# Kernel tuning notes

Measured on AMD Instinct MI355X. Metric: run time of the kernel, lower is better.

Reference implementation:

```python
import jax, jax.numpy as jnp
import numpy as np

NUM_NODES = 15000


def _gcn_conv(x, W, b, src, dst, norm, num_nodes):
    # PyG GCNConv: x' = D^-1/2 (A + I) D^-1/2 (x W) + b
    h = x @ W                                   # [N, out]
    msg = h[src] * norm[:, None]                # gather + scale per edge
    out = jax.ops.segment_sum(msg, dst, num_segments=num_nodes)
    return out + b


def setup_inputs() -> dict:
    key = jax.random.key(0)
    ks = jax.random.split(key, 12)
    T = 100000
    E = 200000
    inp = {
        "x": jax.random.normal(ks[0], (NUM_NODES, 768), jnp.float32),
        "r_emb": jax.random.normal(ks[1], (T, 768), jnp.float32),
        "W1": jax.random.normal(ks[2], (768, 10), jnp.float32) * 0.05,
        "b1": jax.random.normal(ks[3], (10,), jnp.float32) * 0.05,
        "W2": jax.random.normal(ks[4], (10, 128), jnp.float32) * 0.05,
        "b2": jax.random.normal(ks[5], (128,), jnp.float32) * 0.05,
        "W_ih": jax.random.normal(ks[6], (512, 1024), jnp.float32) * 0.03,
        "W_hh": jax.random.normal(ks[7], (512, 128), jnp.float32) * 0.03,
        "b_ih": jax.random.normal(ks[8], (512,), jnp.float32) * 0.03,
        "b_hh": jax.random.normal(ks[9], (512,), jnp.float32) * 0.03,
        "edge_index": jax.random.randint(ks[10], (2, E), 0, NUM_NODES).astype(jnp.int64),
        "triples": jax.random.randint(ks[11], (T, 3), 0, NUM_NODES).astype(jnp.int64),
    }
    return inp


def reference(x, r_emb, W1, b1, W2, b2, W_ih, W_hh, b_ih, b_hh, edge_index, triples):
    N = x.shape[0]
    H = 128  # lstm hidden size
    # --- add self loops, symmetric GCN normalization ---
    loop = jnp.arange(N, dtype=edge_index.dtype)
    src = jnp.concatenate([edge_index[0], loop])
    dst = jnp.concatenate([edge_index[1], loop])
    deg = jax.ops.segment_sum(jnp.ones_like(dst, jnp.float32), dst, num_segments=N)
    dinv = jnp.where(deg > 0, jax.lax.rsqrt(deg), 0.0)
    norm = dinv[src] * dinv[dst]                      # [E+N]
    # --- 2-layer GCN ---
    h = jax.nn.relu(_gcn_conv(x, W1, b1, src, dst, norm, N))   # [N, 10]
    z = _gcn_conv(h, W2, b2, src, dst, norm, N)                # [N, 128]
    # --- per-triple LSTM scoring, batched (seq_len=1, zero init state) ---
    hvec = z[triples[:, 0]]                           # [T, 128]
    tvec = z[triples[:, 2]]                           # [T, 128]
    feat = jnp.concatenate([hvec, r_emb, tvec], axis=-1)       # [T, 1024]
    gates = feat @ W_ih.T + (b_ih + b_hh)             # [T, 512]; h0=0 so W_hh term vanishes
    i_g, f_g, g_g, o_g = jnp.split(gates, 4, axis=-1)  # torch gate order i,f,g,o
    c = jax.nn.sigmoid(i_g) * jnp.tanh(g_g)           # c0 = 0 -> forget term drops
    out = jax.nn.sigmoid(o_g) * jnp.tanh(c)           # [T, 128]
    score = jax.nn.sigmoid(jnp.sum(out, axis=-1))     # [T]
    return score
```

## Files before the change

kernel.cpp:

```cpp
#include <hip/hip_runtime.h>

#define NF 768
#define D1 10
#define D2 128
#define BM 64

typedef __attribute__((ext_vector_type(8))) short bf16x8;
typedef __attribute__((ext_vector_type(16))) float f32x16;

static __device__ __forceinline__ float sigf(float v){ return 1.0f/(1.0f+__expf(-v)); }
static __device__ __forceinline__ float tanhfast(float v){ return 2.0f/(1.0f+__expf(-2.0f*v)) - 1.0f; }
static __device__ __forceinline__ short f2bf(float f){
    unsigned u = __float_as_uint(f);
    u += 0x7fffu + ((u>>16)&1u);
    return (short)(u>>16);
}

__global__ void k_deg(const int* __restrict__ dst, int* __restrict__ cnt, int E){
    int e = blockIdx.x*256 + threadIdx.x;
    if(e<E) atomicAdd(&cnt[dst[e]], 1);
}

__global__ __launch_bounds__(256) void k_scan(const int* __restrict__ cnt,
                                              int* __restrict__ rowptr, int* __restrict__ rowcur,
                                              float* __restrict__ dinv, int N, int E){
    __shared__ int part[256];
    int t = threadIdx.x;
    int C = (N+255)/256;
    int lo = t*C, hi = lo+C; if(hi>N) hi=N; if(lo>N) lo=N;
    int s=0;
    for(int i=lo;i<hi;i++) s += cnt[i];
    part[t]=s;
    __syncthreads();
    if(t==0){
        int run=0;
        for(int i=0;i<256;i++){ int v=part[i]; part[i]=run; run+=v; }
        rowptr[N]=E;
    }
    __syncthreads();
    int run = part[t];
    for(int i=lo;i<hi;i++){
        rowptr[i]=run; rowcur[i]=run; run += cnt[i];
        dinv[i] = rsqrtf((float)cnt[i] + 1.0f);
    }
}

__global__ void k_fill(const int* __restrict__ src, const int* __restrict__ dst,
                       const float* __restrict__ dinv, int* __restrict__ rowcur,
                       int* __restrict__ esrc, float* __restrict__ enorm, int E){
    int e = blockIdx.x*256 + threadIdx.x;
    if(e>=E) return;
    int s=src[e], d=dst[e];
    int pos = atomicAdd(&rowcur[d], 1);
    esrc[pos]=s;
    enorm[pos]=dinv[s]*dinv[d];
}

__global__ __launch_bounds__(256) void k_h1(const float* __restrict__ x,
                                            const float* __restrict__ W1,
                                            float* __restrict__ h1, int N){
    __shared__ float wt[D1*NF];
    for(int idx=threadIdx.x; idx<NF*D1; idx+=256){
        int k=idx/D1, c=idx-k*D1;
        wt[c*NF+k]=W1[idx];
    }
    __syncthreads();
    int row = blockIdx.x*4 + (threadIdx.x>>6);
    int lane = threadIdx.x&63;
    if(row>=N) return;
    const float4* xr = (const float4*)(x + (size_t)row*NF);
    float acc[D1];
#pragma unroll
    for(int c=0;c<D1;c++) acc[c]=0.f;
#pragma unroll
    for(int i=0;i<3;i++){
        float4 v = xr[lane + 64*i];
#pragma unroll
        for(int c=0;c<D1;c++){
            float4 w = *(const float4*)&wt[c*NF + (lane+64*i)*4];
            acc[c] += v.x*w.x + v.y*w.y + v.z*w.z + v.w*w.w;
        }
    }
#pragma unroll
    for(int c=0;c<D1;c++){
        float v=acc[c];
#pragma unroll
        for(int off=32;off;off>>=1) v += __shfl_down(v,off,64);
        acc[c]=v;
    }
    if(lane==0){
#pragma unroll
        for(int c=0;c<D1;c++) h1[(size_t)row*D1+c]=acc[c];
    }
}

__global__ __launch_bounds__(256) void k_gath1(const float* __restrict__ h1,
        const int* __restrict__ rowptr, const int* __restrict__ esrc,
        const float* __restrict__ enorm, const float* __restrict__ dinv,
        const float* __restrict__ b1, float* __restrict__ h, int N){
    int node = blockIdx.x*4 + (threadIdx.x>>6);
    int lane = threadIdx.x&63;
    if(node>=N) return;
    int e0=rowptr[node], e1=rowptr[node+1];
    float acc[D1];
#pragma unroll
    for(int c=0;c<D1;c++) acc[c]=0.f;
    for(int e=e0+lane; e<e1; e+=64){
        int s=esrc[e]; float w=enorm[e];
        const float* hr = h1 + (size_t)s*D1;
#pragma unroll
        for(int c=0;c<D1;c++) acc[c] += hr[c]*w;
    }
    if(lane==0){
        float di=dinv[node], d2=di*di;
        const float* hr = h1 + (size_t)node*D1;
#pragma unroll
        for(int c=0;c<D1;c++) acc[c] += hr[c]*d2;
    }
#pragma unroll
    for(int c=0;c<D1;c++){
        float v=acc[c];
#pragma unroll
        for(int off=32;off;off>>=1) v += __shfl_down(v,off,64);
        acc[c]=v;
    }
    if(lane==0){
#pragma unroll
        for(int c=0;c<D1;c++){
            float v = acc[c] + b1[c];
            h[(size_t)node*D1+c] = v>0.f ? v : 0.f;
        }
    }
}

__global__ __launch_bounds__(128) void k_hz(const float* __restrict__ h,
                                            const float* __restrict__ W2,
                                            float* __restrict__ hz, int N){
    __shared__ float w2s[D1*D2];
    int j = threadIdx.x;
    for(int i=j;i<D1*D2;i+=128) w2s[i]=W2[i];
    __syncthreads();
    int n = blockIdx.x;
    if(n>=N) return;
    const float* hr = h + (size_t)n*D1;
    float acc=0.f;
#pragma unroll
    for(int k=0;k<D1;k++) acc += hr[k]*w2s[k*D2+j];
    hz[(size_t)n*D2+j]=acc;
}

__global__ __launch_bounds__(128) void k_gath2(const float* __restrict__ hz,
        const int* __restrict__ rowptr, const int* __restrict__ esrc,
        const float* __restrict__ enorm, const float* __restrict__ dinv,
        const float* __restrict__ b2, ushort* __restrict__ zb, int N){
    int n = blockIdx.x;
    int c = threadIdx.x;
    int e0 = rowptr[n], e1 = rowptr[n+1];
    float di = dinv[n];
    float acc = hz[(size_t)n*D2+c]*di*di + b2[c];
    int e = e0;
    for(; e+1<e1; e+=2){
        int s0=esrc[e], s1=esrc[e+1];
        float w0=enorm[e], w1=enorm[e+1];
        acc += hz[(size_t)s0*D2+c]*w0 + hz[(size_t)s1*D2+c]*w1;
    }
    if(e<e1) acc += hz[(size_t)esrc[e]*D2+c]*enorm[e];
    zb[(size_t)n*D2+c] = (ushort)f2bf(acc);
}

__global__ void k_wimgB(const float* __restrict__ Wih, ushort* __restrict__ img){
    int gid = blockIdx.x*256 + threadIdx.x;
    if(gid >= 12*64*64) return;
    int l = gid & 63;
    int ks16 = (gid>>6) & 63;
    int f = gid >> 12;
    int dd = l & 31, kb = l>>5;
    int wn = f/3, gi = f - wn*3;
    int gbase = (gi==0)?0:((gi==1)?256:384);
    int wrow = gbase + wn*32 + dd;
    int k = ks16*16 + kb*8;
    const float* p = Wih + (size_t)wrow*1024 + k;
    float4 v0=*(const float4*)p, v1=*(const float4*)(p+4);
    bf16x8 o;
    o[0]=f2bf(v0.x); o[1]=f2bf(v0.y); o[2]=f2bf(v0.z); o[3]=f2bf(v0.w);
    o[4]=f2bf(v1.x); o[5]=f2bf(v1.y); o[6]=f2bf(v1.z); o[7]=f2bf(v1.w);
    *(bf16x8*)(img + (size_t)gid*8) = o;
}

static __device__ __forceinline__ void stage_chunk(ushort* __restrict__ buf, int ch,
        int tid, int t0, int T, const float* __restrict__ remb,
        const ushort* __restrict__ zb, const int* __restrict__ trip){
    int row = tid>>2, q = tid&3;
    int tc = t0+row; if(tc>=T) tc=T-1;
    int xr = row&7;
    ushort* lrow = buf + row*256;
    const size_t rb = (size_t)tc*NF;
#pragma unroll
    for(int j=0;j<8;j++){
        int s = q + 4*j;
        int G = ch*32 + s;
        if(G < 16){
            const ushort* zrow = zb + (size_t)trip[3*tc]*D2;
            *(int4*)(lrow + (s^xr)*8) = *(const int4*)(zrow + G*8);
        } else if(G < 112){
            int g = G-16;
            const float* p = remb + rb + (size_t)g*8;
            float4 v0=*(const float4*)p, v1=*(const float4*)(p+4);
            bf16x8 o;
            o[0]=f2bf(v0.x); o[1]=f2bf(v0.y); o[2]=f2bf(v0.z); o[3]=f2bf(v0.w);
            o[4]=f2bf(v1.x); o[5]=f2bf(v1.y); o[6]=f2bf(v1.z); o[7]=f2bf(v1.w);
            *(bf16x8*)(lrow + (s^xr)*8) = o;
        } else {
            const ushort* zrow = zb + (size_t)trip[3*tc+2]*D2;
            *(int4*)(lrow + (s^xr)*8) = *(const int4*)(zrow + (G-112)*8);
        }
    }
}

__global__ __launch_bounds__(256,2) void k_big(
    const float* __restrict__ remb, const ushort* __restrict__ img,
    const ushort* __restrict__ zb, const float* __restrict__ b_ih,
    const float* __restrict__ b_hh, const int* __restrict__ trip,
    float* __restrict__ score, int T)
{
    __shared__ ushort Abuf[2][64*256];
    int tid=threadIdx.x, lane=tid&63, wn=tid>>6;
    int l31=lane&31, lh=lane>>5;
    int t0=blockIdx.x*BM;

    const ushort* wb0 = img + ((size_t)(wn*3+0)*64*64 + lane)*8;
    const ushort* wb1 = img + ((size_t)(wn*3+1)*64*64 + lane)*8;
    const ushort* wb2 = img + ((size_t)(wn*3+2)*64*64 + lane)*8;
    const int base0 = l31*256;
    const int base1 = (32+l31)*256;
    const int xorm = l31&7;

    f32x16 acc[2][3];
    const f32x16 zer = {0,0,0,0,0,0,0,0,0,0,0,0,0,0,0,0};
#pragma unroll
    for(int m=0;m<2;m++)
#pragma unroll
        for(int g=0;g<3;g++) acc[m][g]=zer;

    stage_chunk(Abuf[0], 0, tid, t0, T, remb, zb, trip);
    __syncthreads();

    for(int ch=0; ch<4; ++ch){
        ushort* cur = Abuf[ch&1];
        if(ch<3) stage_chunk(Abuf[(ch+1)&1], ch+1, tid, t0, T, remb, zb, trip);
        bf16x8 qb[2][3], pa[2][2];
#pragma unroll
        for(int p=0;p<2;p++){
            int ks = ch*16 + p;
            qb[p][0]=*(const bf16x8*)(wb0+(size_t)ks*512);
            qb[p][1]=*(const bf16x8*)(wb1+(size_t)ks*512);
            qb[p][2]=*(const bf16x8*)(wb2+(size_t)ks*512);
            pa[p][0]=*(const bf16x8*)&cur[base0 + ((p*2+lh)^xorm)*8];
            pa[p][1]=*(const bf16x8*)&cur[base1 + ((p*2+lh)^xorm)*8];
        }
#pragma unroll
        for(int c=0;c<16;c++){
            int bs=c&1;
            bf16x8 a0=pa[bs][0], a1=pa[bs][1];
            bf16x8 b0=qb[bs][0], b1=qb[bs][1], b2=qb[bs][2];
            if(c+2<16){
                int ks = ch*16 + c+2;
                qb[bs][0]=*(const bf16x8*)(wb0+(size_t)ks*512);
                qb[bs][1]=*(const bf16x8*)(wb1+(size_t)ks*512);
                qb[bs][2]=*(const bf16x8*)(wb2+(size_t)ks*512);
                pa[bs][0]=*(const bf16x8*)&cur[base0 + (((c+2)*2+lh)^xorm)*8];
                pa[bs][1]=*(const bf16x8*)&cur[base1 + (((c+2)*2+lh)^xorm)*8];
            }
            acc[0][0]=__builtin_amdgcn_mfma_f32_32x32x16_bf16(a0,b0,acc[0][0],0,0,0);
            acc[0][1]=__builtin_amdgcn_mfma_f32_32x32x16_bf16(a0,b1,acc[0][1],0,0,0);
            acc[0][2]=__builtin_amdgcn_mfma_f32_32x32x16_bf16(a0,b2,acc[0][2],0,0,0);
            acc[1][0]=__builtin_amdgcn_mfma_f32_32x32x16_bf16(a1,b0,acc[1][0],0,0,0);
            acc[1][1]=__builtin_amdgcn_mfma_f32_32x32x16_bf16(a1,b1,acc[1][1],0,0,0);
            acc[1][2]=__builtin_amdgcn_mfma_f32_32x32x16_bf16(a1,b2,acc[1][2],0,0,0);
        }
        __syncthreads();
    }

    float* rowsum = (float*)&Abuf[0][0];
    if(tid<BM) rowsum[tid]=0.f;
    __syncthreads();
    int d = wn*32+l31;
    float bi=b_ih[d]+b_hh[d];
    float bg=b_ih[256+d]+b_hh[256+d];
    float bo=b_ih[384+d]+b_hh[384+d];
#pragma unroll
    for(int m=0;m<2;m++){
#pragma unroll
        for(int r=0;r<16;r++){
            int row = m*32 + (r&3)+8*(r>>2)+4*lh;
            float ig = acc[m][0][r] + bi;
            float gg = acc[m][1][r] + bg;
            float og = acc[m][2][r] + bo;
            float cc = sigf(ig)*tanhfast(gg);
            float ov = sigf(og)*tanhfast(cc);
#pragma unroll
            for(int off=1; off<32; off<<=1) ov += __shfl_xor(ov, off, 64);
            if(l31==0) atomicAdd(&rowsum[row], ov);
        }
    }
    __syncthreads();
    if(tid < BM){
        int t = t0 + tid;
        if(t < T) score[t] = sigf(rowsum[tid]);
    }
}

extern "C" void kernel_launch(void* const* d_in, const int* in_sizes, int n_in,
                              void* d_out, int out_size, void* d_ws, size_t ws_size,
                              hipStream_t stream){
    const float* x    = (const float*)d_in[0];
    const float* remb = (const float*)d_in[1];
    const float* W1   = (const float*)d_in[2];
    const float* b1   = (const float*)d_in[3];
    const float* W2   = (const float*)d_in[4];
    const float* b2   = (const float*)d_in[5];
    const float* Wih  = (const float*)d_in[6];
    const float* b_ih = (const float*)d_in[8];
    const float* b_hh = (const float*)d_in[9];
    const int*   ei   = (const int*)d_in[10];
    const int*   trip = (const int*)d_in[11];
    float* score = (float*)d_out;

    const int N = in_sizes[0]/NF;
    const int E = in_sizes[10]/2;
    const int T = in_sizes[11]/3;
    const int* src = ei;
    const int* dst = ei + E;

    float* ws = (float*)d_ws;
    size_t o = 0;
    ushort* img  = (ushort*)(ws+o); o += (size_t)12*64*64*8/2;
    ushort* zb   = (ushort*)(ws+o); o += (size_t)N*D2/2;
    int*   cnt    = (int*)(ws+o);   o += (size_t)((N+8)&~7);
    int*   rowptr = (int*)(ws+o);   o += (size_t)((N+8)&~7);
    int*   rowcur = (int*)(ws+o);   o += (size_t)((N+8)&~7);
    int*   esrc   = (int*)(ws+o);   o += (size_t)E;
    float* enorm  = ws+o;           o += (size_t)E;
    float* dinv   = ws+o;           o += (size_t)((N+7)&~7);
    float* h1     = ws+o;           o += (size_t)N*D1;
    float* hbuf   = ws+o;           o += (size_t)N*D1;
    float* hz     = ws+o;           o += (size_t)N*D2;
    (void)ws_size; (void)n_in; (void)out_size;

    hipMemsetAsync(cnt, 0, (size_t)N*sizeof(int), stream);

    k_wimgB<<<dim3((12*64*64+255)/256), dim3(256), 0, stream>>>(Wih, img);
    k_deg  <<<dim3((E+255)/256), dim3(256), 0, stream>>>(dst, cnt, E);
    k_scan <<<dim3(1), dim3(256), 0, stream>>>(cnt, rowptr, rowcur, dinv, N, E);
    k_fill <<<dim3((E+255)/256), dim3(256), 0, stream>>>(src, dst, dinv, rowcur, esrc, enorm, E);
    k_h1   <<<dim3((N+3)/4), dim3(256), 0, stream>>>(x, W1, h1, N);
    k_gath1<<<dim3((N+3)/4), dim3(256), 0, stream>>>(h1, rowptr, esrc, enorm, dinv, b1, hbuf, N);
    k_hz   <<<dim3(N), dim3(128), 0, stream>>>(hbuf, W2, hz, N);
    k_gath2<<<dim3(N), dim3(128), 0, stream>>>(hz, rowptr, esrc, enorm, dinv, b2, zb, N);
    k_big  <<<dim3((T+BM-1)/BM), dim3(256), 0, stream>>>(remb, img, zb, b_ih, b_hh, trip, score, T);
}
```

Measured before the change: 324.3 us.

## Split A-tile staging into async register loads overlapped with MFMA, reorder LDS layout

The staging of each A chunk is split into an issue phase (global loads into registers) and a write phase (bf16 convert and LDS store). These are interleaved with the two halves of the MFMA loop, so global latency is hidden behind compute. The LDS layout changes to a fragment-major order so each lane reads contiguous 16 bytes with no XOR swizzle. The weight prefetch distance grows from 2 to 4 k-steps and crosses chunk boundaries, and s_setprio raises wave priority during the MFMA bursts. In exchange, register pressure rises from the pending buffers and the deeper B prefetch, which could hurt occupancy under launch_bounds(256,2).

```diff
diff --git a/kernel.cpp b/kernel.cpp
--- a/kernel.cpp
+++ b/kernel.cpp
@@ -187,32 +187,45 @@
     *(bf16x8*)(img + (size_t)gid*8) = o;
 }
 
-static __device__ __forceinline__ void stage_chunk(ushort* __restrict__ buf, int ch,
+struct PendG { float4 lo, hi; };
+
+static __device__ __forceinline__ void issue_groups(PendG* __restrict__ pend, int ch1, int jbase,
         int tid, int t0, int T, const float* __restrict__ remb,
         const ushort* __restrict__ zb, const int* __restrict__ trip){
     int row = tid>>2, q = tid&3;
     int tc = t0+row; if(tc>=T) tc=T-1;
-    int xr = row&7;
-    ushort* lrow = buf + row*256;
-    const size_t rb = (size_t)tc*NF;
-#pragma unroll
-    for(int j=0;j<8;j++){
-        int s = q + 4*j;
-        int G = ch*32 + s;
+#pragma unroll
+    for(int j=0;j<4;j++){
+        int gl = q + 4*(jbase+j);
+        int G = ch1*32 + gl;
         if(G < 16){
-            const ushort* zrow = zb + (size_t)trip[3*tc]*D2;
-            *(int4*)(lrow + (s^xr)*8) = *(const int4*)(zrow + G*8);
+            pend[j].lo = *(const float4*)(zb + (size_t)trip[3*tc]*D2 + G*8);
         } else if(G < 112){
-            int g = G-16;
-            const float* p = remb + rb + (size_t)g*8;
-            float4 v0=*(const float4*)p, v1=*(const float4*)(p+4);
+            const float* p = remb + (size_t)tc*NF + (size_t)(G-16)*8;
+            pend[j].lo = *(const float4*)p;
+            pend[j].hi = *(const float4*)(p+4);
+        } else {
+            pend[j].lo = *(const float4*)(zb + (size_t)trip[3*tc+2]*D2 + (size_t)(G-112)*8);
+        }
+    }
+}
+
+static __device__ __forceinline__ void write_groups(ushort* __restrict__ buf,
+        const PendG* __restrict__ pend, int ch1, int jbase, int tid){
+    int row = tid>>2, q = tid&3;
+    int mb = row>>5, r31 = row&31;
+#pragma unroll
+    for(int j=0;j<4;j++){
+        int gl = q + 4*(jbase+j);
+        int G = ch1*32 + gl;
+        int slot = ((mb*16 + (gl>>1))*64 + r31 + 32*(gl&1))*8;
+        if(G >= 16 && G < 112){
             bf16x8 o;
-            o[0]=f2bf(v0.x); o[1]=f2bf(v0.y); o[2]=f2bf(v0.z); o[3]=f2bf(v0.w);
-            o[4]=f2bf(v1.x); o[5]=f2bf(v1.y); o[6]=f2bf(v1.z); o[7]=f2bf(v1.w);
-            *(bf16x8*)(lrow + (s^xr)*8) = o;
+            o[0]=f2bf(pend[j].lo.x); o[1]=f2bf(pend[j].lo.y); o[2]=f2bf(pend[j].lo.z); o[3]=f2bf(pend[j].lo.w);
+            o[4]=f2bf(pend[j].hi.x); o[5]=f2bf(pend[j].hi.y); o[6]=f2bf(pend[j].hi.z); o[7]=f2bf(pend[j].hi.w);
+            *(bf16x8*)(buf + slot) = o;
         } else {
-            const ushort* zrow = zb + (size_t)trip[3*tc+2]*D2;
-            *(int4*)(lrow + (s^xr)*8) = *(const int4*)(zrow + (G-112)*8);
+            *(float4*)(buf + slot) = pend[j].lo;
         }
     }
 }
@@ -223,7 +236,7 @@
     const float* __restrict__ b_hh, const int* __restrict__ trip,
     float* __restrict__ score, int T)
 {
-    __shared__ ushort Abuf[2][64*256];
+    __shared__ ushort Abuf[2][32*64*8];
     int tid=threadIdx.x, lane=tid&63, wn=tid>>6;
     int l31=lane&31, lh=lane>>5;
     int t0=blockIdx.x*BM;
@@ -231,9 +244,7 @@
     const ushort* wb0 = img + ((size_t)(wn*3+0)*64*64 + lane)*8;
     const ushort* wb1 = img + ((size_t)(wn*3+1)*64*64 + lane)*8;
     const ushort* wb2 = img + ((size_t)(wn*3+2)*64*64 + lane)*8;
-    const int base0 = l31*256;
-    const int base1 = (32+l31)*256;
-    const int xorm = l31&7;
+    const int abase = lane*8;
 
     f32x16 acc[2][3];
     const f32x16 zer = {0,0,0,0,0,0,0,0,0,0,0,0,0,0,0,0};
@@ -242,44 +253,69 @@
 #pragma unroll
         for(int g=0;g<3;g++) acc[m][g]=zer;
 
-    stage_chunk(Abuf[0], 0, tid, t0, T, remb, zb, trip);
-    __syncthreads();
+    bf16x8 qb[4][3];
+#pragma unroll
+    for(int p=0;p<4;p++){
+        qb[p][0]=*(const bf16x8*)(wb0+(size_t)p*512);
+        qb[p][1]=*(const bf16x8*)(wb1+(size_t)p*512);
+        qb[p][2]=*(const bf16x8*)(wb2+(size_t)p*512);
+    }
+
+    PendG pend[4];
+    issue_groups(pend, 0, 0, tid, t0, T, remb, zb, trip);
+    write_groups(Abuf[0], pend, 0, 0, tid);
+    issue_groups(pend, 0, 4, tid, t0, T, remb, zb, trip);
+    write_groups(Abuf[0], pend, 0, 4, tid);
+    __syncthreads();
+
+#define STEP(C_) { \
+        const int bs_=(C_)&3, as_=(C_)&1; \
+        bf16x8 a0=pa[as_][0], a1=pa[as_][1]; \
+        bf16x8 b0=qb[bs_][0], b1=qb[bs_][1], b2v=qb[bs_][2]; \
+        if((C_)+2<16){ \
+            pa[as_][0]=*(const bf16x8*)&cur[((C_)+2)*512 + abase]; \
+            pa[as_][1]=*(const bf16x8*)&cur[(16+(C_)+2)*512 + abase]; \
+        } \
+        if(ch*16+(C_)+4 < 64){ \
+            size_t ko_=(size_t)(ch*16+(C_)+4)*512; \
+            qb[bs_][0]=*(const bf16x8*)(wb0+ko_); \
+            qb[bs_][1]=*(const bf16x8*)(wb1+ko_); \
+            qb[bs_][2]=*(const bf16x8*)(wb2+ko_); \
+        } \
+        acc[0][0]=__builtin_amdgcn_mfma_f32_32x32x16_bf16(a0,b0 ,acc[0][0],0,0,0); \
+        acc[0][1]=__builtin_amdgcn_mfma_f32_32x32x16_bf16(a0,b1 ,acc[0][1],0,0,0); \
+        acc[0][2]=__builtin_amdgcn_mfma_f32_32x32x16_bf16(a0,b2v,acc[0][2],0,0,0); \
+        acc[1][0]=__builtin_amdgcn_mfma_f32_32x32x16_bf16(a1,b0 ,acc[1][0],0,0,0); \
+        acc[1][1]=__builtin_amdgcn_mfma_f32_32x32x16_bf16(a1,b1 ,acc[1][1],0,0,0); \
+        acc[1][2]=__builtin_amdgcn_mfma_f32_32x32x16_bf16(a1,b2v,acc[1][2],0,0,0); \
+    }
 
     for(int ch=0; ch<4; ++ch){
         ushort* cur = Abuf[ch&1];
-        if(ch<3) stage_chunk(Abuf[(ch+1)&1], ch+1, tid, t0, T, remb, zb, trip);
-        bf16x8 qb[2][3], pa[2][2];
-#pragma unroll
-        for(int p=0;p<2;p++){
-            int ks = ch*16 + p;
-            qb[p][0]=*(const bf16x8*)(wb0+(size_t)ks*512);
-            qb[p][1]=*(const bf16x8*)(wb1+(size_t)ks*512);
-            qb[p][2]=*(const bf16x8*)(wb2+(size_t)ks*512);
-            pa[p][0]=*(const bf16x8*)&cur[base0 + ((p*2+lh)^xorm)*8];
-            pa[p][1]=*(const bf16x8*)&cur[base1 + ((p*2+lh)^xorm)*8];
-        }
-#pragma unroll
-        for(int c=0;c<16;c++){
-            int bs=c&1;
-            bf16x8 a0=pa[bs][0], a1=pa[bs][1];
-            bf16x8 b0=qb[bs][0], b1=qb[bs][1], b2=qb[bs][2];
-            if(c+2<16){
-                int ks = ch*16 + c+2;
-                qb[bs][0]=*(const bf16x8*)(wb0+(size_t)ks*512);
-                qb[bs][1]=*(const bf16x8*)(wb1+(size_t)ks*512);
-                qb[bs][2]=*(const bf16x8*)(wb2+(size_t)ks*512);
-                pa[bs][0]=*(const bf16x8*)&cur[base0 + (((c+2)*2+lh)^xorm)*8];
-                pa[bs][1]=*(const bf16x8*)&cur[base1 + (((c+2)*2+lh)^xorm)*8];
-            }
-            acc[0][0]=__builtin_amdgcn_mfma_f32_32x32x16_bf16(a0,b0,acc[0][0],0,0,0);
-            acc[0][1]=__builtin_amdgcn_mfma_f32_32x32x16_bf16(a0,b1,acc[0][1],0,0,0);
-            acc[0][2]=__builtin_amdgcn_mfma_f32_32x32x16_bf16(a0,b2,acc[0][2],0,0,0);
-            acc[1][0]=__builtin_amdgcn_mfma_f32_32x32x16_bf16(a1,b0,acc[1][0],0,0,0);
-            acc[1][1]=__builtin_amdgcn_mfma_f32_32x32x16_bf16(a1,b1,acc[1][1],0,0,0);
-            acc[1][2]=__builtin_amdgcn_mfma_f32_32x32x16_bf16(a1,b2,acc[1][2],0,0,0);
-        }
+        ushort* nxt = Abuf[(ch+1)&1];
+        const bool more = (ch<3);
+        if(more) issue_groups(pend, ch+1, 0, tid, t0, T, remb, zb, trip);
+        bf16x8 pa[2][2];
+        pa[0][0]=*(const bf16x8*)&cur[0*512 + abase];
+        pa[0][1]=*(const bf16x8*)&cur[16*512 + abase];
+        pa[1][0]=*(const bf16x8*)&cur[1*512 + abase];
+        pa[1][1]=*(const bf16x8*)&cur[17*512 + abase];
+        __builtin_amdgcn_s_setprio(1);
+#pragma unroll
+        for(int c=0;c<8;c++) STEP(c)
+        __builtin_amdgcn_s_setprio(0);
+        if(more){
+            write_groups(nxt, pend, ch+1, 0, tid);
+            issue_groups(pend, ch+1, 4, tid, t0, T, remb, zb, trip);
+        }
+        __builtin_amdgcn_s_setprio(1);
+#pragma unroll
+        for(int c=8;c<16;c++) STEP(c)
+        __builtin_amdgcn_s_setprio(0);
+        if(more) write_groups(nxt, pend, ch+1, 4, tid);
         __syncthreads();
     }
+#undef STEP
 
     float* rowsum = (float*)&Abuf[0][0];
     if(tid<BM) rowsum[tid]=0.f;
```

New measurement: 396.1 us. +22.1%, slower.

## Stage fp32 activations via async global-to-LDS loads in a 4-deep ring

Applied to the files above, without the earlier changes.

The main LSTM GEMM kernel now stages raw fp32 rows of the gathered node embeddings and r_emb straight into shared memory with global_load_lds. They go into a 4-slot ring of 16 chunks that keeps three chunks in flight. Conversion to bf16 moves to after the LDS read, using packed v_cvt_pk_bf16_f32 instructions. The GCN output is kept in fp32 so all A operands share one path. This aims to hide memory latency and take register-staged conversion off the load path, at the cost of more LDS traffic (fp32 is twice the bf16 size) and hand-tuned waitcnt and barrier scheduling.

```diff
diff --git a/kernel.cpp b/kernel.cpp
--- a/kernel.cpp
+++ b/kernel.cpp
@@ -14,6 +14,24 @@
     unsigned u = __float_as_uint(f);
     u += 0x7fffu + ((u>>16)&1u);
     return (short)(u>>16);
+}
+
+static __device__ __forceinline__ void gload16(const void* g, void* l){
+    __builtin_amdgcn_global_load_lds(
+        (const __attribute__((address_space(1))) unsigned int*)(unsigned long long)g,
+        (__attribute__((address_space(3))) unsigned int*)(unsigned long long)l,
+        16, 0, 0);
+}
+
+static __device__ __forceinline__ bf16x8 cvt8(float4 a, float4 b){
+    unsigned u0,u1,u2,u3;
+    asm("v_cvt_pk_bf16_f32 %0, %1, %2" : "=v"(u0) : "v"(a.x), "v"(a.y));
+    asm("v_cvt_pk_bf16_f32 %0, %1, %2" : "=v"(u1) : "v"(a.z), "v"(a.w));
+    asm("v_cvt_pk_bf16_f32 %0, %1, %2" : "=v"(u2) : "v"(b.x), "v"(b.y));
+    asm("v_cvt_pk_bf16_f32 %0, %1, %2" : "=v"(u3) : "v"(b.z), "v"(b.w));
+    union { unsigned u[4]; bf16x8 v; } r;
+    r.u[0]=u0; r.u[1]=u1; r.u[2]=u2; r.u[3]=u3;
+    return r.v;
 }
 
 __global__ void k_deg(const int* __restrict__ dst, int* __restrict__ cnt, int E){
@@ -152,7 +170,7 @@
 __global__ __launch_bounds__(128) void k_gath2(const float* __restrict__ hz,
         const int* __restrict__ rowptr, const int* __restrict__ esrc,
         const float* __restrict__ enorm, const float* __restrict__ dinv,
-        const float* __restrict__ b2, ushort* __restrict__ zb, int N){
+        const float* __restrict__ b2, float* __restrict__ zbf, int N){
     int n = blockIdx.x;
     int c = threadIdx.x;
     int e0 = rowptr[n], e1 = rowptr[n+1];
@@ -165,7 +183,7 @@
         acc += hz[(size_t)s0*D2+c]*w0 + hz[(size_t)s1*D2+c]*w1;
     }
     if(e<e1) acc += hz[(size_t)esrc[e]*D2+c]*enorm[e];
-    zb[(size_t)n*D2+c] = (ushort)f2bf(acc);
+    zbf[(size_t)n*D2+c] = acc;
 }
 
 __global__ void k_wimgB(const float* __restrict__ Wih, ushort* __restrict__ img){
@@ -187,53 +205,36 @@
     *(bf16x8*)(img + (size_t)gid*8) = o;
 }
 
-static __device__ __forceinline__ void stage_chunk(ushort* __restrict__ buf, int ch,
-        int tid, int t0, int T, const float* __restrict__ remb,
-        const ushort* __restrict__ zb, const int* __restrict__ trip){
-    int row = tid>>2, q = tid&3;
-    int tc = t0+row; if(tc>=T) tc=T-1;
-    int xr = row&7;
-    ushort* lrow = buf + row*256;
-    const size_t rb = (size_t)tc*NF;
-#pragma unroll
-    for(int j=0;j<8;j++){
-        int s = q + 4*j;
-        int G = ch*32 + s;
-        if(G < 16){
-            const ushort* zrow = zb + (size_t)trip[3*tc]*D2;
-            *(int4*)(lrow + (s^xr)*8) = *(const int4*)(zrow + G*8);
-        } else if(G < 112){
-            int g = G-16;
-            const float* p = remb + rb + (size_t)g*8;
-            float4 v0=*(const float4*)p, v1=*(const float4*)(p+4);
-            bf16x8 o;
-            o[0]=f2bf(v0.x); o[1]=f2bf(v0.y); o[2]=f2bf(v0.z); o[3]=f2bf(v0.w);
-            o[4]=f2bf(v1.x); o[5]=f2bf(v1.y); o[6]=f2bf(v1.z); o[7]=f2bf(v1.w);
-            *(bf16x8*)(lrow + (s^xr)*8) = o;
-        } else {
-            const ushort* zrow = zb + (size_t)trip[3*tc+2]*D2;
-            *(int4*)(lrow + (s^xr)*8) = *(const int4*)(zrow + (G-112)*8);
-        }
-    }
-}
-
 __global__ __launch_bounds__(256,2) void k_big(
     const float* __restrict__ remb, const ushort* __restrict__ img,
-    const ushort* __restrict__ zb, const float* __restrict__ b_ih,
+    const float* __restrict__ zbf, const float* __restrict__ b_ih,
     const float* __restrict__ b_hh, const int* __restrict__ trip,
     float* __restrict__ score, int T)
 {
-    __shared__ ushort Abuf[2][64*256];
-    int tid=threadIdx.x, lane=tid&63, wn=tid>>6;
+    __shared__ float ring[4][64*64];
+    int tid=threadIdx.x, lane=tid&63, w=tid>>6;
     int l31=lane&31, lh=lane>>5;
     int t0=blockIdx.x*BM;
 
-    const ushort* wb0 = img + ((size_t)(wn*3+0)*64*64 + lane)*8;
-    const ushort* wb1 = img + ((size_t)(wn*3+1)*64*64 + lane)*8;
-    const ushort* wb2 = img + ((size_t)(wn*3+2)*64*64 + lane)*8;
-    const int base0 = l31*256;
-    const int base1 = (32+l31)*256;
-    const int xorm = l31&7;
+    const int l16 = lane>>4;
+    size_t rbo[4]; const float* zh4[4]; const float* zt4[4]; int lsl[4];
+#pragma unroll
+    for(int j=0;j<4;j++){
+        int row = w*16 + j*4 + l16;
+        int tc = t0 + row; if(tc>=T) tc=T-1;
+        rbo[j] = (size_t)tc*NF;
+        int th = trip[3*tc], tt = trip[3*tc+2];
+        zh4[j] = zbf + (size_t)th*D2;
+        zt4[j] = zbf + (size_t)tt*D2;
+        lsl[j] = ((lane&15) ^ (row&15))*4;
+    }
+
+    const ushort* wb0 = img + ((size_t)(w*3+0)*64*64 + lane)*8;
+    const ushort* wb1 = img + ((size_t)(w*3+1)*64*64 + lane)*8;
+    const ushort* wb2 = img + ((size_t)(w*3+2)*64*64 + lane)*8;
+    const int base0 = l31*64;
+    const int base1 = (32+l31)*64;
+    const int rx = lane&15;
 
     f32x16 acc[2][3];
     const f32x16 zer = {0,0,0,0,0,0,0,0,0,0,0,0,0,0,0,0};
@@ -242,49 +243,68 @@
 #pragma unroll
         for(int g=0;g<3;g++) acc[m][g]=zer;
 
-    stage_chunk(Abuf[0], 0, tid, t0, T, remb, zb, trip);
-    __syncthreads();
-
-    for(int ch=0; ch<4; ++ch){
-        ushort* cur = Abuf[ch&1];
-        if(ch<3) stage_chunk(Abuf[(ch+1)&1], ch+1, tid, t0, T, remb, zb, trip);
-        bf16x8 qb[2][3], pa[2][2];
-#pragma unroll
-        for(int p=0;p<2;p++){
-            int ks = ch*16 + p;
-            qb[p][0]=*(const bf16x8*)(wb0+(size_t)ks*512);
-            qb[p][1]=*(const bf16x8*)(wb1+(size_t)ks*512);
-            qb[p][2]=*(const bf16x8*)(wb2+(size_t)ks*512);
-            pa[p][0]=*(const bf16x8*)&cur[base0 + ((p*2+lh)^xorm)*8];
-            pa[p][1]=*(const bf16x8*)&cur[base1 + ((p*2+lh)^xorm)*8];
-        }
-#pragma unroll
-        for(int c=0;c<16;c++){
-            int bs=c&1;
-            bf16x8 a0=pa[bs][0], a1=pa[bs][1];
-            bf16x8 b0=qb[bs][0], b1=qb[bs][1], b2=qb[bs][2];
-            if(c+2<16){
-                int ks = ch*16 + c+2;
-                qb[bs][0]=*(const bf16x8*)(wb0+(size_t)ks*512);
-                qb[bs][1]=*(const bf16x8*)(wb1+(size_t)ks*512);
-                qb[bs][2]=*(const bf16x8*)(wb2+(size_t)ks*512);
-                pa[bs][0]=*(const bf16x8*)&cur[base0 + (((c+2)*2+lh)^xorm)*8];
-                pa[bs][1]=*(const bf16x8*)&cur[base1 + (((c+2)*2+lh)^xorm)*8];
-            }
-            acc[0][0]=__builtin_amdgcn_mfma_f32_32x32x16_bf16(a0,b0,acc[0][0],0,0,0);
-            acc[0][1]=__builtin_amdgcn_mfma_f32_32x32x16_bf16(a0,b1,acc[0][1],0,0,0);
-            acc[0][2]=__builtin_amdgcn_mfma_f32_32x32x16_bf16(a0,b2,acc[0][2],0,0,0);
-            acc[1][0]=__builtin_amdgcn_mfma_f32_32x32x16_bf16(a1,b0,acc[1][0],0,0,0);
-            acc[1][1]=__builtin_amdgcn_mfma_f32_32x32x16_bf16(a1,b1,acc[1][1],0,0,0);
-            acc[1][2]=__builtin_amdgcn_mfma_f32_32x32x16_bf16(a1,b2,acc[1][2],0,0,0);
-        }
-        __syncthreads();
-    }
-
-    float* rowsum = (float*)&Abuf[0][0];
+#define ISSUE(C_) { \
+    float* dst_ = &ring[(C_)&3][(w*16)*64]; \
+    _Pragma("unroll") \
+    for(int j_=0;j_<4;j_++){ \
+        const float* src_; \
+        if((C_)<2)       src_ = zh4[j_] + (C_)*64 + lsl[j_]; \
+        else if((C_)<14) src_ = remb + rbo[j_] + ((C_)-2)*64 + lsl[j_]; \
+        else             src_ = zt4[j_] + ((C_)-14)*64 + lsl[j_]; \
+        gload16(src_, dst_ + j_*4*64); \
+    } }
+
+    ISSUE(0) ISSUE(1) ISSUE(2)
+    bf16x8 qb[2][3];
+    qb[0][0]=*(const bf16x8*)(wb0);     qb[0][1]=*(const bf16x8*)(wb1);     qb[0][2]=*(const bf16x8*)(wb2);
+    qb[1][0]=*(const bf16x8*)(wb0+512); qb[1][1]=*(const bf16x8*)(wb1+512); qb[1][2]=*(const bf16x8*)(wb2+512);
+
+#define KSTEP(C_,S_) { \
+    const float4 a00_ = *(const float4*)&cur_[base0 + ((((S_)*4+lh*2)  )^rx)*4]; \
+    const float4 a01_ = *(const float4*)&cur_[base0 + ((((S_)*4+lh*2)+1)^rx)*4]; \
+    const float4 a10_ = *(const float4*)&cur_[base1 + ((((S_)*4+lh*2)  )^rx)*4]; \
+    const float4 a11_ = *(const float4*)&cur_[base1 + ((((S_)*4+lh*2)+1)^rx)*4]; \
+    bf16x8 A0_ = cvt8(a00_, a01_); \
+    bf16x8 A1_ = cvt8(a10_, a11_); \
+    bf16x8 B0_=qb[(S_)&1][0], B1_=qb[(S_)&1][1], B2_=qb[(S_)&1][2]; \
+    if((C_)*4+(S_)+2 < 64){ \
+        size_t ko_ = (size_t)((C_)*4+(S_)+2)*512; \
+        qb[(S_)&1][0]=*(const bf16x8*)(wb0+ko_); \
+        qb[(S_)&1][1]=*(const bf16x8*)(wb1+ko_); \
+        qb[(S_)&1][2]=*(const bf16x8*)(wb2+ko_); \
+    } \
+    acc[0][0]=__builtin_amdgcn_mfma_f32_32x32x16_bf16(A0_,B0_,acc[0][0],0,0,0); \
+    acc[0][1]=__builtin_amdgcn_mfma_f32_32x32x16_bf16(A0_,B1_,acc[0][1],0,0,0); \
+    acc[0][2]=__builtin_amdgcn_mfma_f32_32x32x16_bf16(A0_,B2_,acc[0][2],0,0,0); \
+    acc[1][0]=__builtin_amdgcn_mfma_f32_32x32x16_bf16(A1_,B0_,acc[1][0],0,0,0); \
+    acc[1][1]=__builtin_amdgcn_mfma_f32_32x32x16_bf16(A1_,B1_,acc[1][1],0,0,0); \
+    acc[1][2]=__builtin_amdgcn_mfma_f32_32x32x16_bf16(A1_,B2_,acc[1][2],0,0,0); \
+}
+
+#define CHUNK(C_) { \
+    asm volatile("s_waitcnt vmcnt(12)" ::: "memory"); \
+    __builtin_amdgcn_s_barrier(); \
+    __builtin_amdgcn_sched_barrier(0); \
+    if((C_)+3 < 16) { ISSUE((C_)+3) } \
+    const float* cur_ = &ring[(C_)&3][0]; \
+    __builtin_amdgcn_s_setprio(1); \
+    KSTEP(C_,0) KSTEP(C_,1) KSTEP(C_,2) KSTEP(C_,3) \
+    __builtin_amdgcn_s_setprio(0); \
+}
+
+    CHUNK(0)  CHUNK(1)  CHUNK(2)  CHUNK(3)
+    CHUNK(4)  CHUNK(5)  CHUNK(6)  CHUNK(7)
+    CHUNK(8)  CHUNK(9)  CHUNK(10) CHUNK(11)
+    CHUNK(12) CHUNK(13) CHUNK(14) CHUNK(15)
+#undef CHUNK
+#undef KSTEP
+#undef ISSUE
+
+    float* rowsum = &ring[0][0];
+    __syncthreads();
     if(tid<BM) rowsum[tid]=0.f;
     __syncthreads();
-    int d = wn*32+l31;
+    int d = w*32+l31;
     float bi=b_ih[d]+b_hh[d];
     float bg=b_ih[256+d]+b_hh[256+d];
     float bo=b_ih[384+d]+b_hh[384+d];
@@ -335,7 +355,7 @@
     float* ws = (float*)d_ws;
     size_t o = 0;
     ushort* img  = (ushort*)(ws+o); o += (size_t)12*64*64*8/2;
-    ushort* zb   = (ushort*)(ws+o); o += (size_t)N*D2/2;
+    float* zbf   = ws+o;            o += (size_t)N*D2;
     int*   cnt    = (int*)(ws+o);   o += (size_t)((N+8)&~7);
     int*   rowptr = (int*)(ws+o);   o += (size_t)((N+8)&~7);
     int*   rowcur = (int*)(ws+o);   o += (size_t)((N+8)&~7);
@@ -356,6 +376,6 @@
     k_h1   <<<dim3((N+3)/4), dim3(256), 0, stream>>>(x, W1, h1, N);
     k_gath1<<<dim3((N+3)/4), dim3(256), 0, stream>>>(h1, rowptr, esrc, enorm, dinv, b1, hbuf, N);
     k_hz   <<<dim3(N), dim3(128), 0, stream>>>(hbuf, W2, hz, N);
-    k_gath2<<<dim3(N), dim3(128), 0, stream>>>(hz, rowptr, esrc, enorm, dinv, b2, zb, N);
-    k_big  <<<dim3((T+BM-1)/BM), dim3(256), 0, stream>>>(remb, img, zb, b_ih, b_hh, trip, score, T);
-}
+    k_gath2<<<dim3(N), dim3(128), 0, stream>>>(hz, rowptr, esrc, enorm, dinv, b2, zbf, N);
+    k_big  <<<dim3((T+BM-1)/BM), dim3(256), 0, stream>>>(remb, img, zbf, b_ih, b_hh, trip, score, T);
+}
```

After: 316.3 us. -2.5%, faster.
